# Performance work log

Hardware: AMD Instinct MI355X
Metric: run time of the kernel (lower is better)

The kernel has to match this reference:

```python
import jax, jax.numpy as jnp
import numpy as np

N = 100000
E = 2000000
IN_DIM = 5
D = 32
L = 3
EPS = 1e-5


def setup_inputs() -> dict:
    key = jax.random.key(0)
    ks = jax.random.split(key, 10)
    x = jax.random.normal(ks[0], (N, IN_DIM), dtype=jnp.float32)
    edge_index = jax.random.randint(ks[1], (2, E), 0, N, dtype=jnp.int64)
    s = 1.0 / np.sqrt(D)
    w_in = jax.random.normal(ks[2], (D, IN_DIM), dtype=jnp.float32) / np.sqrt(IN_DIM)
    b_in = jnp.zeros((D,), dtype=jnp.float32)
    w_l = jax.random.normal(ks[3], (L, D, D), dtype=jnp.float32) * s  # lin_l per layer
    b_l = jnp.zeros((L, D), dtype=jnp.float32)
    w_r = jax.random.normal(ks[4], (L, D, D), dtype=jnp.float32) * s  # lin_r per layer (no bias, as in PyG SAGEConv)
    gamma = jnp.ones((D,), dtype=jnp.float32)
    beta = jnp.zeros((D,), dtype=jnp.float32)
    return {"x": x, "edge_index": edge_index, "w_in": w_in, "b_in": b_in,
            "w_l": w_l, "b_l": b_l, "w_r": w_r, "gamma": gamma, "beta": beta}


def _layernorm(h, gamma, beta):
    mu = jnp.mean(h, axis=-1, keepdims=True)
    var = jnp.mean(jnp.square(h - mu), axis=-1, keepdims=True)
    return (h - mu) * jax.lax.rsqrt(var + EPS) * gamma + beta


def reference(x, edge_index, w_in, b_in, w_l, b_l, w_r, gamma, beta):
    src = edge_index[0]
    dst = edge_index[1]
    n = x.shape[0]
    # node in-degree for mean aggregation (0-degree nodes get 0 output, like scatter_mean)
    deg = jax.ops.segment_sum(jnp.ones((src.shape[0],), dtype=x.dtype), dst, num_segments=n)
    inv_deg = (1.0 / jnp.maximum(deg, 1.0))[:, None]  # [N,1]
    h = x @ w_in.T + b_in  # [N, D]
    for i in range(w_l.shape[0]):
        msg = h[src]  # [E, D] gather
        agg = jax.ops.segment_sum(msg, dst, num_segments=n) * inv_deg  # mean aggregate
        h = agg @ w_l[i].T + b_l[i] + h @ w_r[i].T  # SAGEConv: lin_l(aggr) + lin_r(x)
        h = _layernorm(jax.nn.relu(h), gamma, beta)
    return h
```

## Files before the change

### kernel.cpp

```cpp
#include <hip/hip_runtime.h>
#include <hip/hip_bf16.h>

#define DIM 32
#define INDIM 5
#define EPB 4096
#define BKBITS 7
#define BKN 128
#define NBMAX 1024
#define CAP 4096

__device__ __forceinline__ unsigned short f2bf(float f) {
    unsigned u = __float_as_uint(f);
    u += 0x7FFFu + ((u >> 16) & 1u);
    return (unsigned short)(u >> 16);
}
__device__ __forceinline__ float bf2f_lo(unsigned u) { return __uint_as_float(u << 16); }
__device__ __forceinline__ float bf2f_hi(unsigned u) { return __uint_as_float(u & 0xFFFF0000u); }

__device__ __forceinline__ void acc_pk(float2& a01, float2& a23, float2& a45, float2& a67,
                                       uint4 v) {
    float2 v01, v23, v45, v67;
    v01.x = bf2f_lo(v.x); v01.y = bf2f_hi(v.x);
    v23.x = bf2f_lo(v.y); v23.y = bf2f_hi(v.y);
    v45.x = bf2f_lo(v.z); v45.y = bf2f_hi(v.z);
    v67.x = bf2f_lo(v.w); v67.y = bf2f_hi(v.w);
    asm volatile("v_pk_add_f32 %0, %0, %1" : "+v"(a01) : "v"(v01));
    asm volatile("v_pk_add_f32 %0, %0, %1" : "+v"(a23) : "v"(v23));
    asm volatile("v_pk_add_f32 %0, %0, %1" : "+v"(a45) : "v"(v45));
    asm volatile("v_pk_add_f32 %0, %0, %1" : "+v"(a67) : "v"(v67));
}


__global__ __launch_bounds__(256) void bucket_count_kernel(const int* __restrict__ dst,
                                                           int* __restrict__ bcnt, int e, int nb) {
    __shared__ int hist[NBMAX];
    int t = threadIdx.x;
    for (int i = t; i < nb; i += 256) hist[i] = 0;
    __syncthreads();
    int base = blockIdx.x * EPB;
    for (int k = 0; k < EPB; k += 256) {
        int i = base + k + t;
        if (i < e) {
            int dv = __builtin_nontemporal_load(&dst[i]);
            atomicAdd(&hist[dv >> BKBITS], 1);
        }
    }
    __syncthreads();
    for (int i = t; i < nb; i += 256) {
        int h = hist[i];
        if (h) atomicAdd(&bcnt[i], h);
    }
}


__global__ void bucket_scan_kernel(const int* __restrict__ bcnt, int* __restrict__ bbase,
                                   int* __restrict__ bcur, int* __restrict__ row_ptr,
                                   int nb, int n, int e) {
    __shared__ int s[1024];
    int t = threadIdx.x;
    int v = (t < nb) ? bcnt[t] : 0;
    s[t] = v;
    __syncthreads();
    for (int o = 1; o < 1024; o <<= 1) {
        int a = (t >= o) ? s[t - o] : 0;
        __syncthreads();
        s[t] += a;
        __syncthreads();
    }
    if (t < nb) {
        int excl = s[t] - v;
        bbase[t] = excl;
        bcur[t] = excl;
    }
    if (t == 0) {
        bbase[nb] = e;
        row_ptr[n] = e;
    }
}


__global__ __launch_bounds__(256) void bucket_fill_kernel(const int* __restrict__ src,
                                                          const int* __restrict__ dst,
                                                          int* __restrict__ bcur,
                                                          unsigned* __restrict__ packed,
                                                          int e, int nb) {
    __shared__ unsigned sw[EPB];
    __shared__ unsigned short sb[EPB];
    __shared__ int hist[NBMAX];
    __shared__ int rbase[NBMAX];
    int t = threadIdx.x;
    for (int i = t; i < nb; i += 256) hist[i] = 0;
    __syncthreads();
    int base = blockIdx.x * EPB;
    for (int k = 0; k < EPB; k += 256) {
        int i = base + k + t;
        if (i < e) {
            int s = __builtin_nontemporal_load(&src[i]);
            int d = __builtin_nontemporal_load(&dst[i]);
            int b = d >> BKBITS;
            sw[k + t] = ((unsigned)s << BKBITS) | (unsigned)(d & (BKN - 1));
            sb[k + t] = (unsigned short)b;
            atomicAdd(&hist[b], 1);
        }
    }
    __syncthreads();
    for (int i = t; i < nb; i += 256) {
        int h = hist[i];
        rbase[i] = h ? atomicAdd(&bcur[i], h) : 0;
        hist[i] = 0;
    }
    __syncthreads();
    for (int k = 0; k < EPB; k += 256) {
        int i = base + k + t;
        if (i < e) {
            int b = sb[k + t];
            int r = atomicAdd(&hist[b], 1);
            packed[rbase[b] + r] = sw[k + t];
        }
    }
}


__global__ __launch_bounds__(256) void csr_build_kernel(const unsigned* __restrict__ packed,
                                                        const int* __restrict__ bbase,
                                                        int* __restrict__ row_ptr,
                                                        int* __restrict__ esrc, int n) {
    __shared__ unsigned ew[CAP];
    __shared__ int h2[BKN];
    __shared__ int off[BKN];
    int b = blockIdx.x;
    int base = bbase[b];
    int cnt = bbase[b + 1] - base;
    int t = threadIdx.x;
    if (t < BKN) h2[t] = 0;
    __syncthreads();
    bool staged = (cnt <= CAP);
    for (int i = t; i < cnt; i += 256) {
        unsigned w = __builtin_nontemporal_load(&packed[base + i]);
        if (staged) ew[i] = w;
        atomicAdd(&h2[w & (BKN - 1)], 1);
    }
    __syncthreads();
    int v = 0;
    if (t < BKN) {
        v = h2[t];
        off[t] = v;
    }
    __syncthreads();
    for (int o = 1; o < BKN; o <<= 1) {
        int a = 0;
        if (t < BKN && t >= o) a = off[t - o];
        __syncthreads();
        if (t < BKN) off[t] += a;
        __syncthreads();
    }
    if (t < BKN) {
        int excl = off[t] - v;
        off[t] = excl;
        h2[t] = 0;
    }
    __syncthreads();
    int node = b * BKN + t;
    if (t < BKN && node < n) row_ptr[node] = base + off[t];
    for (int i = t; i < cnt; i += 256) {
        unsigned w = staged ? ew[i] : packed[base + i];
        int dl = w & (BKN - 1);
        int r = atomicAdd(&h2[dl], 1);
        esrc[base + off[dl] + r] = (int)(w >> BKBITS);
    }
}


__global__ void input_proj_kernel(const float* __restrict__ x, const float* __restrict__ w_in,
                                  const float* __restrict__ b_in,
                                  unsigned short* __restrict__ h, int n) {
    __shared__ float sw[DIM * INDIM];
    __shared__ float sb[DIM];
    int t = threadIdx.x;
    if (t < DIM * INDIM) sw[t] = w_in[t];
    if (t < DIM) sb[t] = b_in[t];
    __syncthreads();
    int idx = blockIdx.x * 256 + t;
    int node = idx >> 5;
    int d = idx & 31;
    if (node < n) {
        const float* xr = x + (size_t)node * INDIM;
        float acc = sb[d];
#pragma unroll
        for (int k = 0; k < INDIM; k++) acc = fmaf(xr[k], sw[d * INDIM + k], acc);
        h[(size_t)node * DIM + d] = f2bf(acc);
    }
}


template <int LAST>
__global__ __launch_bounds__(64, 4) void layer_fused_kernel(
    const int* __restrict__ row_ptr, const int* __restrict__ esrc,
    const unsigned short* __restrict__ h_in,
    unsigned short* __restrict__ h_out_bf, float* __restrict__ out_f32,
    const float* __restrict__ wl, const float* __restrict__ bl,
    const float* __restrict__ wr, const float* __restrict__ gamma,
    const float* __restrict__ beta, int n) {
    __shared__ float sAgg[16][DIM];
    __shared__ float sSelf[16][DIM];

    int t = threadIdx.x;
    int d = t & 31;

    int nd = t >> 2;
    int q = t & 3;
    int node = blockIdx.x * 16 + nd;
    const uint4* hv = (const uint4*)h_in;

    if (node < n) {
        {
            uint4 v = hv[(size_t)node * 4 + q];
            float4 f0 = make_float4(bf2f_lo(v.x), bf2f_hi(v.x), bf2f_lo(v.y), bf2f_hi(v.y));
            float4 f1 = make_float4(bf2f_lo(v.z), bf2f_hi(v.z), bf2f_lo(v.w), bf2f_hi(v.w));
            *(float4*)&sSelf[nd][q * 8] = f0;
            *(float4*)&sSelf[nd][q * 8 + 4] = f1;
        }
        int rs = row_ptr[node];
        int re = row_ptr[node + 1];
        float2 a01 = make_float2(0.f, 0.f), a23 = make_float2(0.f, 0.f);
        float2 a45 = make_float2(0.f, 0.f), a67 = make_float2(0.f, 0.f);
        int j = rs;
        for (; j + 16 <= re; j += 16) {
            int ids[16];
#pragma unroll
            for (int k = 0; k < 16; k++) ids[k] = __builtin_nontemporal_load(&esrc[j + k]);
            uint4 vv[16];
#pragma unroll
            for (int k = 0; k < 16; k++) vv[k] = hv[(size_t)ids[k] * 4 + q];
#pragma unroll
            for (int k = 0; k < 16; k++) acc_pk(a01, a23, a45, a67, vv[k]);
        }
        if (j < re) {
            int m = re - j;
            int ids[16];
#pragma unroll
            for (int k = 0; k < 16; k++) ids[k] = (k < m) ? __builtin_nontemporal_load(&esrc[j + k]) : 0;
            uint4 vv[16];
#pragma unroll
            for (int k = 0; k < 16; k++) vv[k] = hv[(size_t)ids[k] * 4 + q];
#pragma unroll
            for (int k = 0; k < 16; k++) {
                uint4 v = vv[k];
                if (k >= m) { v.x = 0u; v.y = 0u; v.z = 0u; v.w = 0u; }
                acc_pk(a01, a23, a45, a67, v);
            }
        }
        float iv = 1.f / fmaxf((float)(re - rs), 1.f);
        float4 f0 = make_float4(a01.x * iv, a01.y * iv, a23.x * iv, a23.y * iv);
        float4 f1 = make_float4(a45.x * iv, a45.y * iv, a67.x * iv, a67.y * iv);
        *(float4*)&sAgg[nd][q * 8] = f0;
        *(float4*)&sAgg[nd][q * 8 + 4] = f1;
    }
    __syncthreads();

    float wlr[DIM], wrr[DIM];
    {
        const float4* p1 = (const float4*)(wl + (size_t)d * DIM);
        const float4* p2 = (const float4*)(wr + (size_t)d * DIM);
#pragma unroll
        for (int qq = 0; qq < 8; qq++) {
            float4 a = p1[qq];
            wlr[4 * qq] = a.x; wlr[4 * qq + 1] = a.y; wlr[4 * qq + 2] = a.z; wlr[4 * qq + 3] = a.w;
            float4 c = p2[qq];
            wrr[4 * qq] = c.x; wrr[4 * qq + 1] = c.y; wrr[4 * qq + 2] = c.z; wrr[4 * qq + 3] = c.w;
        }
    }
    float bias = bl[d], g = gamma[d], be = beta[d];

#pragma unroll
    for (int it = 0; it < 8; ++it) {
        int ln = it * 2 + (t >> 5);
        int nodec = blockIdx.x * 16 + ln;
        if (nodec < n) {
            float o = bias;
            const float* va = sAgg[ln];
            const float* vs = sSelf[ln];
#pragma unroll
            for (int qq = 0; qq < 8; qq++) {
                float4 a = *(const float4*)&va[qq * 4];
                float4 s = *(const float4*)&vs[qq * 4];
                o = fmaf(a.x, wlr[4 * qq], o);     o = fmaf(s.x, wrr[4 * qq], o);
                o = fmaf(a.y, wlr[4 * qq + 1], o); o = fmaf(s.y, wrr[4 * qq + 1], o);
                o = fmaf(a.z, wlr[4 * qq + 2], o); o = fmaf(s.z, wrr[4 * qq + 2], o);
                o = fmaf(a.w, wlr[4 * qq + 3], o); o = fmaf(s.w, wrr[4 * qq + 3], o);
            }
            float out = fmaxf(o, 0.f);
            float sum = out, sq = out * out;
#pragma unroll
            for (int off = 16; off > 0; off >>= 1) {
                sum += __shfl_xor(sum, off, 32);
                sq += __shfl_xor(sq, off, 32);
            }
            float mu = sum * (1.f / 32.f);
            float var = fmaxf(sq * (1.f / 32.f) - mu * mu, 0.f);
            float r = rsqrtf(var + 1e-5f);
            float res = (out - mu) * r * g + be;
            if (LAST) __builtin_nontemporal_store(res, &out_f32[(size_t)nodec * DIM + d]);
            else      __builtin_nontemporal_store(f2bf(res), &h_out_bf[(size_t)nodec * DIM + d]);
        }
    }
}


extern "C" void kernel_launch(void* const* d_in, const int* in_sizes, int n_in,
                              void* d_out, int out_size, void* d_ws, size_t ws_size,
                              hipStream_t stream) {
    const float* x = (const float*)d_in[0];
    const int* ei = (const int*)d_in[1];
    const float* w_in = (const float*)d_in[2];
    const float* b_in = (const float*)d_in[3];
    const float* w_l = (const float*)d_in[4];
    const float* b_l = (const float*)d_in[5];
    const float* w_r = (const float*)d_in[6];
    const float* gamma = (const float*)d_in[7];
    const float* beta = (const float*)d_in[8];

    int n = in_sizes[0] / INDIM;
    int e = in_sizes[1] / 2;
    int L = in_sizes[4] / (DIM * DIM);
    const int* src = ei;
    const int* dst = ei + e;
    int nb = (n + BKN - 1) >> BKBITS;

    char* w = (char*)d_ws;
    int* bcnt = (int*)w;               w += (size_t)NBMAX * 4;
    int* bbase = (int*)w;              w += (size_t)(NBMAX + 1) * 4;
    int* bcur = (int*)w;               w += (size_t)NBMAX * 4;
    int* row_ptr = (int*)w;            w += (size_t)(n + 1) * 4;
    int* esrc = (int*)w;               w += (size_t)e * 4;
    unsigned short* h_A = (unsigned short*)w;  w += (size_t)n * DIM * 2;
    unsigned short* h_B = (unsigned short*)w;  w += (size_t)n * DIM * 2;
    unsigned* packed = (unsigned*)h_A;

    int nbE = (e + EPB - 1) / EPB;

    hipMemsetAsync(bcnt, 0, (size_t)nb * 4, stream);
    bucket_count_kernel<<<nbE, 256, 0, stream>>>(dst, bcnt, e, nb);
    bucket_scan_kernel<<<1, 1024, 0, stream>>>(bcnt, bbase, bcur, row_ptr, nb, n, e);
    bucket_fill_kernel<<<nbE, 256, 0, stream>>>(src, dst, bcur, packed, e, nb);
    csr_build_kernel<<<nb, 256, 0, stream>>>(packed, bbase, row_ptr, esrc, n);

    input_proj_kernel<<<(n * DIM + 255) / 256, 256, 0, stream>>>(x, w_in, b_in, h_A, n);

    unsigned short* bufs[2] = {h_A, h_B};
    int nbF = (n + 15) / 16;
    for (int i = 0; i < L; i++) {
        const unsigned short* hin = bufs[i & 1];
        unsigned short* hout = bufs[(i + 1) & 1];
        const float* wl = w_l + (size_t)i * DIM * DIM;
        const float* bl = b_l + (size_t)i * DIM;
        const float* wr = w_r + (size_t)i * DIM * DIM;
        if (i == L - 1)
            layer_fused_kernel<1><<<nbF, 64, 0, stream>>>(row_ptr, esrc, hin, nullptr,
                                                          (float*)d_out, wl, bl, wr,
                                                          gamma, beta, n);
        else
            layer_fused_kernel<0><<<nbF, 64, 0, stream>>>(row_ptr, esrc, hin, hout,
                                                          nullptr, wl, bl, wr,
                                                          gamma, beta, n);
    }
}
```

Baseline: 254.5 us.

## Split node features into two half-planes and gather each in a separate pass

Node features are now stored as two planes, dims 0-15 and dims 16-31, each 3.2 MB in bf16. Each layer runs two gather passes: one accumulates the low half into an fp32 scratch buffer, the other accumulates the high half and then does the fused linear, ReLU and LayerNorm step. The goal is to shrink the random-gather working set so each pass fits better in cache. The cost is reading the CSR edge list twice per layer, an extra kernel launch, and an fp32 round trip for the partial aggregates. Block size also doubles to 32 nodes, and the nontemporal loads and stores are dropped.

```diff
diff --git a/kernel.cpp b/kernel.cpp
--- a/kernel.cpp
+++ b/kernel.cpp
@@ -17,17 +17,12 @@
 __device__ __forceinline__ float bf2f_lo(unsigned u) { return __uint_as_float(u << 16); }
 __device__ __forceinline__ float bf2f_hi(unsigned u) { return __uint_as_float(u & 0xFFFF0000u); }
 
-__device__ __forceinline__ void acc_pk(float2& a01, float2& a23, float2& a45, float2& a67,
-                                       uint4 v) {
-    float2 v01, v23, v45, v67;
+__device__ __forceinline__ void acc_pk2(float2& a01, float2& a23, uint2 v) {
+    float2 v01, v23;
     v01.x = bf2f_lo(v.x); v01.y = bf2f_hi(v.x);
     v23.x = bf2f_lo(v.y); v23.y = bf2f_hi(v.y);
-    v45.x = bf2f_lo(v.z); v45.y = bf2f_hi(v.z);
-    v67.x = bf2f_lo(v.w); v67.y = bf2f_hi(v.w);
     asm volatile("v_pk_add_f32 %0, %0, %1" : "+v"(a01) : "v"(v01));
     asm volatile("v_pk_add_f32 %0, %0, %1" : "+v"(a23) : "v"(v23));
-    asm volatile("v_pk_add_f32 %0, %0, %1" : "+v"(a45) : "v"(v45));
-    asm volatile("v_pk_add_f32 %0, %0, %1" : "+v"(a67) : "v"(v67));
 }
 
 
@@ -188,73 +183,112 @@
         float acc = sb[d];
 #pragma unroll
         for (int k = 0; k < INDIM; k++) acc = fmaf(xr[k], sw[d * INDIM + k], acc);
-        h[(size_t)node * DIM + d] = f2bf(acc);
-    }
+        h[(size_t)(d >> 4) * n * 16 + (size_t)node * 16 + (d & 15)] = f2bf(acc);
+    }
+}
+
+
+__global__ __launch_bounds__(128, 4) void gather_lo_kernel(
+    const int* __restrict__ row_ptr, const int* __restrict__ esrc,
+    const unsigned short* __restrict__ h_in, float* __restrict__ aggs, int n) {
+    int t = threadIdx.x;
+    int nd = t >> 2, q = t & 3;
+    int node = blockIdx.x * 32 + nd;
+    if (node >= n) return;
+    const uint2* hv = (const uint2*)h_in;
+    int rs = row_ptr[node], re = row_ptr[node + 1];
+    float2 a01 = make_float2(0.f, 0.f), a23 = make_float2(0.f, 0.f);
+    int j = rs;
+    for (; j + 16 <= re; j += 16) {
+        int ids[16];
+#pragma unroll
+        for (int k = 0; k < 16; k++) ids[k] = esrc[j + k];
+        uint2 vv[16];
+#pragma unroll
+        for (int k = 0; k < 16; k++) vv[k] = hv[(size_t)ids[k] * 4 + q];
+#pragma unroll
+        for (int k = 0; k < 16; k++) acc_pk2(a01, a23, vv[k]);
+    }
+    if (j < re) {
+        int m = re - j;
+        int ids[16];
+#pragma unroll
+        for (int k = 0; k < 16; k++) ids[k] = (k < m) ? esrc[j + k] : 0;
+        uint2 vv[16];
+#pragma unroll
+        for (int k = 0; k < 16; k++) vv[k] = hv[(size_t)ids[k] * 4 + q];
+#pragma unroll
+        for (int k = 0; k < 16; k++) {
+            uint2 v = vv[k];
+            if (k >= m) { v.x = 0u; v.y = 0u; }
+            acc_pk2(a01, a23, v);
+        }
+    }
+    *(float4*)&aggs[(size_t)node * 16 + q * 4] = make_float4(a01.x, a01.y, a23.x, a23.y);
 }
 
 
 template <int LAST>
-__global__ __launch_bounds__(64, 4) void layer_fused_kernel(
+__global__ __launch_bounds__(128, 3) void layer_hi_kernel(
     const int* __restrict__ row_ptr, const int* __restrict__ esrc,
-    const unsigned short* __restrict__ h_in,
+    const unsigned short* __restrict__ h_in, const float* __restrict__ aggs,
     unsigned short* __restrict__ h_out_bf, float* __restrict__ out_f32,
     const float* __restrict__ wl, const float* __restrict__ bl,
     const float* __restrict__ wr, const float* __restrict__ gamma,
     const float* __restrict__ beta, int n) {
-    __shared__ float sAgg[16][DIM];
-    __shared__ float sSelf[16][DIM];
+    __shared__ float sAgg[32][DIM];
+    __shared__ float sSelf[32][DIM];
 
     int t = threadIdx.x;
     int d = t & 31;
-
-    int nd = t >> 2;
-    int q = t & 3;
-    int node = blockIdx.x * 16 + nd;
-    const uint4* hv = (const uint4*)h_in;
+    int nd = t >> 2, q = t & 3;
+    int node = blockIdx.x * 32 + nd;
+    const uint2* hvlo = (const uint2*)h_in;
+    const uint2* hvhi = (const uint2*)(h_in + (size_t)n * 16);
 
     if (node < n) {
         {
-            uint4 v = hv[(size_t)node * 4 + q];
-            float4 f0 = make_float4(bf2f_lo(v.x), bf2f_hi(v.x), bf2f_lo(v.y), bf2f_hi(v.y));
-            float4 f1 = make_float4(bf2f_lo(v.z), bf2f_hi(v.z), bf2f_lo(v.w), bf2f_hi(v.w));
-            *(float4*)&sSelf[nd][q * 8] = f0;
-            *(float4*)&sSelf[nd][q * 8 + 4] = f1;
-        }
-        int rs = row_ptr[node];
-        int re = row_ptr[node + 1];
+            uint2 slo = hvlo[(size_t)node * 4 + q];
+            uint2 shi = hvhi[(size_t)node * 4 + q];
+            *(float4*)&sSelf[nd][q * 4] =
+                make_float4(bf2f_lo(slo.x), bf2f_hi(slo.x), bf2f_lo(slo.y), bf2f_hi(slo.y));
+            *(float4*)&sSelf[nd][16 + q * 4] =
+                make_float4(bf2f_lo(shi.x), bf2f_hi(shi.x), bf2f_lo(shi.y), bf2f_hi(shi.y));
+        }
+        int rs = row_ptr[node], re = row_ptr[node + 1];
         float2 a01 = make_float2(0.f, 0.f), a23 = make_float2(0.f, 0.f);
-        float2 a45 = make_float2(0.f, 0.f), a67 = make_float2(0.f, 0.f);
         int j = rs;
         for (; j + 16 <= re; j += 16) {
             int ids[16];
 #pragma unroll
-            for (int k = 0; k < 16; k++) ids[k] = __builtin_nontemporal_load(&esrc[j + k]);
-            uint4 vv[16];
-#pragma unroll
-            for (int k = 0; k < 16; k++) vv[k] = hv[(size_t)ids[k] * 4 + q];
-#pragma unroll
-            for (int k = 0; k < 16; k++) acc_pk(a01, a23, a45, a67, vv[k]);
+            for (int k = 0; k < 16; k++) ids[k] = esrc[j + k];
+            uint2 vv[16];
+#pragma unroll
+            for (int k = 0; k < 16; k++) vv[k] = hvhi[(size_t)ids[k] * 4 + q];
+#pragma unroll
+            for (int k = 0; k < 16; k++) acc_pk2(a01, a23, vv[k]);
         }
         if (j < re) {
             int m = re - j;
             int ids[16];
 #pragma unroll
-            for (int k = 0; k < 16; k++) ids[k] = (k < m) ? __builtin_nontemporal_load(&esrc[j + k]) : 0;
-            uint4 vv[16];
-#pragma unroll
-            for (int k = 0; k < 16; k++) vv[k] = hv[(size_t)ids[k] * 4 + q];
+            for (int k = 0; k < 16; k++) ids[k] = (k < m) ? esrc[j + k] : 0;
+            uint2 vv[16];
+#pragma unroll
+            for (int k = 0; k < 16; k++) vv[k] = hvhi[(size_t)ids[k] * 4 + q];
 #pragma unroll
             for (int k = 0; k < 16; k++) {
-                uint4 v = vv[k];
-                if (k >= m) { v.x = 0u; v.y = 0u; v.z = 0u; v.w = 0u; }
-                acc_pk(a01, a23, a45, a67, v);
+                uint2 v = vv[k];
+                if (k >= m) { v.x = 0u; v.y = 0u; }
+                acc_pk2(a01, a23, v);
             }
         }
         float iv = 1.f / fmaxf((float)(re - rs), 1.f);
-        float4 f0 = make_float4(a01.x * iv, a01.y * iv, a23.x * iv, a23.y * iv);
-        float4 f1 = make_float4(a45.x * iv, a45.y * iv, a67.x * iv, a67.y * iv);
-        *(float4*)&sAgg[nd][q * 8] = f0;
-        *(float4*)&sAgg[nd][q * 8 + 4] = f1;
+        float4 lo4 = *(const float4*)&aggs[(size_t)node * 16 + q * 4];
+        *(float4*)&sAgg[nd][q * 4] =
+            make_float4(lo4.x * iv, lo4.y * iv, lo4.z * iv, lo4.w * iv);
+        *(float4*)&sAgg[nd][16 + q * 4] =
+            make_float4(a01.x * iv, a01.y * iv, a23.x * iv, a23.y * iv);
     }
     __syncthreads();
 
@@ -274,8 +308,8 @@
 
 #pragma unroll
     for (int it = 0; it < 8; ++it) {
-        int ln = it * 2 + (t >> 5);
-        int nodec = blockIdx.x * 16 + ln;
+        int ln = it * 4 + (t >> 5);
+        int nodec = blockIdx.x * 32 + ln;
         if (nodec < n) {
             float o = bias;
             const float* va = sAgg[ln];
@@ -300,8 +334,8 @@
             float var = fmaxf(sq * (1.f / 32.f) - mu * mu, 0.f);
             float r = rsqrtf(var + 1e-5f);
             float res = (out - mu) * r * g + be;
-            if (LAST) __builtin_nontemporal_store(res, &out_f32[(size_t)nodec * DIM + d]);
-            else      __builtin_nontemporal_store(f2bf(res), &h_out_bf[(size_t)nodec * DIM + d]);
+            if (LAST) out_f32[(size_t)nodec * DIM + d] = res;
+            else      h_out_bf[(size_t)(d >> 4) * n * 16 + (size_t)nodec * 16 + (d & 15)] = f2bf(res);
         }
     }
 }
@@ -333,6 +367,7 @@
     int* bcur = (int*)w;               w += (size_t)NBMAX * 4;
     int* row_ptr = (int*)w;            w += (size_t)(n + 1) * 4;
     int* esrc = (int*)w;               w += (size_t)e * 4;
+    float* aggs = (float*)w;           w += (size_t)n * 16 * 4;
     unsigned short* h_A = (unsigned short*)w;  w += (size_t)n * DIM * 2;
     unsigned short* h_B = (unsigned short*)w;  w += (size_t)n * DIM * 2;
     unsigned* packed = (unsigned*)h_A;
@@ -348,20 +383,21 @@
     input_proj_kernel<<<(n * DIM + 255) / 256, 256, 0, stream>>>(x, w_in, b_in, h_A, n);
 
     unsigned short* bufs[2] = {h_A, h_B};
-    int nbF = (n + 15) / 16;
+    int nbF = (n + 31) / 32;
     for (int i = 0; i < L; i++) {
         const unsigned short* hin = bufs[i & 1];
         unsigned short* hout = bufs[(i + 1) & 1];
         const float* wl = w_l + (size_t)i * DIM * DIM;
         const float* bl = b_l + (size_t)i * DIM;
         const float* wr = w_r + (size_t)i * DIM * DIM;
+        gather_lo_kernel<<<nbF, 128, 0, stream>>>(row_ptr, esrc, hin, aggs, n);
         if (i == L - 1)
-            layer_fused_kernel<1><<<nbF, 64, 0, stream>>>(row_ptr, esrc, hin, nullptr,
-                                                          (float*)d_out, wl, bl, wr,
-                                                          gamma, beta, n);
+            layer_hi_kernel<1><<<nbF, 128, 0, stream>>>(row_ptr, esrc, hin, aggs, nullptr,
+                                                        (float*)d_out, wl, bl, wr,
+                                                        gamma, beta, n);
         else
-            layer_fused_kernel<0><<<nbF, 64, 0, stream>>>(row_ptr, esrc, hin, hout,
-                                                          nullptr, wl, bl, wr,
-                                                          gamma, beta, n);
-    }
-}
+            layer_hi_kernel<0><<<nbF, 128, 0, stream>>>(row_ptr, esrc, hin, aggs, hout,
+                                                        nullptr, wl, bl, wr,
+                                                        gamma, beta, n);
+    }
+}
```

After: 276.2 us. +8.5%, slower.

## Split neighbor gather into two passes by source-node half for L2 locality

Applied to the files above, without the earlier changes.

The CSR build now sorts each destination row's edges by whether the source node is in the lower or upper half of the node range, and records a per-node midpoint. Each layer becomes two kernels: one gathers and sums the lower-half sources into an fp32 scratch buffer (d_out reused as scratch), and one gathers the upper-half sources, adds the partial sum, and does the fused linear, ReLU and LayerNorm. The aim is to shrink each pass's random-gather working set to about half the feature table so it stays cache-resident. The cost is an extra launch per layer and an fp32 partial-aggregate write and read per node. Block size also grows to 32 nodes, and nontemporal hints on edge loads and output stores are removed.

```diff
diff --git a/kernel.cpp b/kernel.cpp
--- a/kernel.cpp
+++ b/kernel.cpp
@@ -124,49 +124,50 @@
 __global__ __launch_bounds__(256) void csr_build_kernel(const unsigned* __restrict__ packed,
                                                         const int* __restrict__ bbase,
                                                         int* __restrict__ row_ptr,
-                                                        int* __restrict__ esrc, int n) {
+                                                        int* __restrict__ row_mid,
+                                                        int* __restrict__ esrc, int n, int nhalf) {
     __shared__ unsigned ew[CAP];
-    __shared__ int h2[BKN];
-    __shared__ int off[BKN];
+    __shared__ int h2[256];
+    __shared__ int off[256];
     int b = blockIdx.x;
     int base = bbase[b];
     int cnt = bbase[b + 1] - base;
     int t = threadIdx.x;
-    if (t < BKN) h2[t] = 0;
+    h2[t] = 0;
     __syncthreads();
     bool staged = (cnt <= CAP);
     for (int i = t; i < cnt; i += 256) {
         unsigned w = __builtin_nontemporal_load(&packed[base + i]);
         if (staged) ew[i] = w;
-        atomicAdd(&h2[w & (BKN - 1)], 1);
-    }
-    __syncthreads();
-    int v = 0;
+        int key = ((w & (BKN - 1)) << 1) | ((int)(w >> BKBITS) >= nhalf ? 1 : 0);
+        atomicAdd(&h2[key], 1);
+    }
+    __syncthreads();
+    int v = h2[t];
+    off[t] = v;
+    __syncthreads();
+    for (int o = 1; o < 256; o <<= 1) {
+        int a = (t >= o) ? off[t - o] : 0;
+        __syncthreads();
+        off[t] += a;
+        __syncthreads();
+    }
+    off[t] -= v;
+    h2[t] = 0;
+    __syncthreads();
     if (t < BKN) {
-        v = h2[t];
-        off[t] = v;
-    }
-    __syncthreads();
-    for (int o = 1; o < BKN; o <<= 1) {
-        int a = 0;
-        if (t < BKN && t >= o) a = off[t - o];
-        __syncthreads();
-        if (t < BKN) off[t] += a;
-        __syncthreads();
-    }
-    if (t < BKN) {
-        int excl = off[t] - v;
-        off[t] = excl;
-        h2[t] = 0;
-    }
-    __syncthreads();
-    int node = b * BKN + t;
-    if (t < BKN && node < n) row_ptr[node] = base + off[t];
+        int node = b * BKN + t;
+        if (node < n) {
+            row_ptr[node] = base + off[2 * t];
+            row_mid[node] = base + off[2 * t + 1];
+        }
+    }
     for (int i = t; i < cnt; i += 256) {
         unsigned w = staged ? ew[i] : packed[base + i];
-        int dl = w & (BKN - 1);
-        int r = atomicAdd(&h2[dl], 1);
-        esrc[base + off[dl] + r] = (int)(w >> BKBITS);
+        int srcv = (int)(w >> BKBITS);
+        int key = ((w & (BKN - 1)) << 1) | (srcv >= nhalf ? 1 : 0);
+        int r = atomicAdd(&h2[key], 1);
+        esrc[base + off[key] + r] = srcv;
     }
 }
 
@@ -193,42 +194,84 @@
 }
 
 
+__global__ __launch_bounds__(128, 4) void gather_lo_kernel(
+    const int* __restrict__ row_ptr, const int* __restrict__ row_mid,
+    const int* __restrict__ esrc, const unsigned short* __restrict__ h_in,
+    float* __restrict__ aggs, int n) {
+    int t = threadIdx.x;
+    int nd = t >> 2, q = t & 3;
+    int node = blockIdx.x * 32 + nd;
+    if (node >= n) return;
+    const uint4* hv = (const uint4*)h_in;
+    int rs = row_ptr[node], mid = row_mid[node];
+    float2 a01 = make_float2(0.f, 0.f), a23 = make_float2(0.f, 0.f);
+    float2 a45 = make_float2(0.f, 0.f), a67 = make_float2(0.f, 0.f);
+    int j = rs;
+    for (; j + 16 <= mid; j += 16) {
+        int ids[16];
+#pragma unroll
+        for (int k = 0; k < 16; k++) ids[k] = esrc[j + k];
+        uint4 vv[16];
+#pragma unroll
+        for (int k = 0; k < 16; k++) vv[k] = hv[(size_t)ids[k] * 4 + q];
+#pragma unroll
+        for (int k = 0; k < 16; k++) acc_pk(a01, a23, a45, a67, vv[k]);
+    }
+    if (j < mid) {
+        int m = mid - j;
+        int ids[16];
+#pragma unroll
+        for (int k = 0; k < 16; k++) ids[k] = (k < m) ? esrc[j + k] : 0;
+        uint4 vv[16];
+#pragma unroll
+        for (int k = 0; k < 16; k++) vv[k] = hv[(size_t)ids[k] * 4 + q];
+#pragma unroll
+        for (int k = 0; k < 16; k++) {
+            uint4 v = vv[k];
+            if (k >= m) { v.x = 0u; v.y = 0u; v.z = 0u; v.w = 0u; }
+            acc_pk(a01, a23, a45, a67, v);
+        }
+    }
+    float* ap = aggs + (size_t)node * DIM + q * 8;
+    *(float4*)(ap) = make_float4(a01.x, a01.y, a23.x, a23.y);
+    *(float4*)(ap + 4) = make_float4(a45.x, a45.y, a67.x, a67.y);
+}
+
+
 template <int LAST>
-__global__ __launch_bounds__(64, 4) void layer_fused_kernel(
-    const int* __restrict__ row_ptr, const int* __restrict__ esrc,
-    const unsigned short* __restrict__ h_in,
+__global__ __launch_bounds__(128, 3) void layer_hi_kernel(
+    const int* __restrict__ row_ptr, const int* __restrict__ row_mid,
+    const int* __restrict__ esrc, const unsigned short* __restrict__ h_in,
+    const float* __restrict__ aggs,
     unsigned short* __restrict__ h_out_bf, float* __restrict__ out_f32,
     const float* __restrict__ wl, const float* __restrict__ bl,
     const float* __restrict__ wr, const float* __restrict__ gamma,
     const float* __restrict__ beta, int n) {
-    __shared__ float sAgg[16][DIM];
-    __shared__ float sSelf[16][DIM];
+    __shared__ float sAgg[32][DIM];
+    __shared__ float sSelf[32][DIM];
 
     int t = threadIdx.x;
     int d = t & 31;
-
-    int nd = t >> 2;
-    int q = t & 3;
-    int node = blockIdx.x * 16 + nd;
+    int nd = t >> 2, q = t & 3;
+    int node = blockIdx.x * 32 + nd;
     const uint4* hv = (const uint4*)h_in;
 
     if (node < n) {
         {
             uint4 v = hv[(size_t)node * 4 + q];
-            float4 f0 = make_float4(bf2f_lo(v.x), bf2f_hi(v.x), bf2f_lo(v.y), bf2f_hi(v.y));
-            float4 f1 = make_float4(bf2f_lo(v.z), bf2f_hi(v.z), bf2f_lo(v.w), bf2f_hi(v.w));
-            *(float4*)&sSelf[nd][q * 8] = f0;
-            *(float4*)&sSelf[nd][q * 8 + 4] = f1;
-        }
-        int rs = row_ptr[node];
-        int re = row_ptr[node + 1];
+            *(float4*)&sSelf[nd][q * 8] =
+                make_float4(bf2f_lo(v.x), bf2f_hi(v.x), bf2f_lo(v.y), bf2f_hi(v.y));
+            *(float4*)&sSelf[nd][q * 8 + 4] =
+                make_float4(bf2f_lo(v.z), bf2f_hi(v.z), bf2f_lo(v.w), bf2f_hi(v.w));
+        }
+        int rs = row_ptr[node], mid = row_mid[node], re = row_ptr[node + 1];
         float2 a01 = make_float2(0.f, 0.f), a23 = make_float2(0.f, 0.f);
         float2 a45 = make_float2(0.f, 0.f), a67 = make_float2(0.f, 0.f);
-        int j = rs;
+        int j = mid;
         for (; j + 16 <= re; j += 16) {
             int ids[16];
 #pragma unroll
-            for (int k = 0; k < 16; k++) ids[k] = __builtin_nontemporal_load(&esrc[j + k]);
+            for (int k = 0; k < 16; k++) ids[k] = esrc[j + k];
             uint4 vv[16];
 #pragma unroll
             for (int k = 0; k < 16; k++) vv[k] = hv[(size_t)ids[k] * 4 + q];
@@ -239,7 +282,7 @@
             int m = re - j;
             int ids[16];
 #pragma unroll
-            for (int k = 0; k < 16; k++) ids[k] = (k < m) ? __builtin_nontemporal_load(&esrc[j + k]) : 0;
+            for (int k = 0; k < 16; k++) ids[k] = (k < m) ? esrc[j + k] : 0;
             uint4 vv[16];
 #pragma unroll
             for (int k = 0; k < 16; k++) vv[k] = hv[(size_t)ids[k] * 4 + q];
@@ -251,10 +294,13 @@
             }
         }
         float iv = 1.f / fmaxf((float)(re - rs), 1.f);
-        float4 f0 = make_float4(a01.x * iv, a01.y * iv, a23.x * iv, a23.y * iv);
-        float4 f1 = make_float4(a45.x * iv, a45.y * iv, a67.x * iv, a67.y * iv);
-        *(float4*)&sAgg[nd][q * 8] = f0;
-        *(float4*)&sAgg[nd][q * 8 + 4] = f1;
+        const float* ap = aggs + (size_t)node * DIM + q * 8;
+        float4 lo0 = *(const float4*)(ap);
+        float4 lo1 = *(const float4*)(ap + 4);
+        *(float4*)&sAgg[nd][q * 8] = make_float4((lo0.x + a01.x) * iv, (lo0.y + a01.y) * iv,
+                                                 (lo0.z + a23.x) * iv, (lo0.w + a23.y) * iv);
+        *(float4*)&sAgg[nd][q * 8 + 4] = make_float4((lo1.x + a45.x) * iv, (lo1.y + a45.y) * iv,
+                                                     (lo1.z + a67.x) * iv, (lo1.w + a67.y) * iv);
     }
     __syncthreads();
 
@@ -274,8 +320,8 @@
 
 #pragma unroll
     for (int it = 0; it < 8; ++it) {
-        int ln = it * 2 + (t >> 5);
-        int nodec = blockIdx.x * 16 + ln;
+        int ln = it * 4 + (t >> 5);
+        int nodec = blockIdx.x * 32 + ln;
         if (nodec < n) {
             float o = bias;
             const float* va = sAgg[ln];
@@ -300,8 +346,8 @@
             float var = fmaxf(sq * (1.f / 32.f) - mu * mu, 0.f);
             float r = rsqrtf(var + 1e-5f);
             float res = (out - mu) * r * g + be;
-            if (LAST) __builtin_nontemporal_store(res, &out_f32[(size_t)nodec * DIM + d]);
-            else      __builtin_nontemporal_store(f2bf(res), &h_out_bf[(size_t)nodec * DIM + d]);
+            if (LAST) out_f32[(size_t)nodec * DIM + d] = res;
+            else      h_out_bf[(size_t)nodec * DIM + d] = f2bf(res);
         }
     }
 }
@@ -326,16 +372,19 @@
     const int* src = ei;
     const int* dst = ei + e;
     int nb = (n + BKN - 1) >> BKBITS;
+    int nhalf = n >> 1;
 
     char* w = (char*)d_ws;
     int* bcnt = (int*)w;               w += (size_t)NBMAX * 4;
     int* bbase = (int*)w;              w += (size_t)(NBMAX + 1) * 4;
     int* bcur = (int*)w;               w += (size_t)NBMAX * 4;
     int* row_ptr = (int*)w;            w += (size_t)(n + 1) * 4;
+    int* row_mid = (int*)w;            w += (size_t)n * 4;
     int* esrc = (int*)w;               w += (size_t)e * 4;
     unsigned short* h_A = (unsigned short*)w;  w += (size_t)n * DIM * 2;
     unsigned short* h_B = (unsigned short*)w;  w += (size_t)n * DIM * 2;
     unsigned* packed = (unsigned*)h_A;
+    float* aggs = (float*)d_out;
 
     int nbE = (e + EPB - 1) / EPB;
 
@@ -343,25 +392,26 @@
     bucket_count_kernel<<<nbE, 256, 0, stream>>>(dst, bcnt, e, nb);
     bucket_scan_kernel<<<1, 1024, 0, stream>>>(bcnt, bbase, bcur, row_ptr, nb, n, e);
     bucket_fill_kernel<<<nbE, 256, 0, stream>>>(src, dst, bcur, packed, e, nb);
-    csr_build_kernel<<<nb, 256, 0, stream>>>(packed, bbase, row_ptr, esrc, n);
+    csr_build_kernel<<<nb, 256, 0, stream>>>(packed, bbase, row_ptr, row_mid, esrc, n, nhalf);
 
     input_proj_kernel<<<(n * DIM + 255) / 256, 256, 0, stream>>>(x, w_in, b_in, h_A, n);
 
     unsigned short* bufs[2] = {h_A, h_B};
-    int nbF = (n + 15) / 16;
+    int nbF = (n + 31) / 32;
     for (int i = 0; i < L; i++) {
         const unsigned short* hin = bufs[i & 1];
         unsigned short* hout = bufs[(i + 1) & 1];
         const float* wl = w_l + (size_t)i * DIM * DIM;
         const float* bl = b_l + (size_t)i * DIM;
         const float* wr = w_r + (size_t)i * DIM * DIM;
+        gather_lo_kernel<<<nbF, 128, 0, stream>>>(row_ptr, row_mid, esrc, hin, aggs, n);
         if (i == L - 1)
-            layer_fused_kernel<1><<<nbF, 64, 0, stream>>>(row_ptr, esrc, hin, nullptr,
-                                                          (float*)d_out, wl, bl, wr,
-                                                          gamma, beta, n);
+            layer_hi_kernel<1><<<nbF, 128, 0, stream>>>(row_ptr, row_mid, esrc, hin, aggs,
+                                                        nullptr, (float*)d_out, wl, bl, wr,
+                                                        gamma, beta, n);
         else
-            layer_fused_kernel<0><<<nbF, 64, 0, stream>>>(row_ptr, esrc, hin, hout,
-                                                          nullptr, wl, bl, wr,
-                                                          gamma, beta, n);
-    }
-}
+            layer_hi_kernel<0><<<nbF, 128, 0, stream>>>(row_ptr, row_mid, esrc, hin, aggs,
+                                                        hout, nullptr, wl, bl, wr,
+                                                        gamma, beta, n);
+    }
+}
```

New measurement: 258.8 us. Within noise of the previous version (+1.7%).
